# Kernel tuning notes

Hardware: AMD Instinct MI355X
Metric: run time of the kernel (lower is better)

Reference implementation:

```python
import jax, jax.numpy as jnp
import numpy as np

N_EMBED = 8192
EMBED_DIM = 256
DECAY = 0.99
EPS = 1e-05


def setup_inputs() -> dict:
    key = jax.random.key(0)
    k1, k2 = jax.random.split(key)
    z = jax.random.normal(k1, (16, 32, 32, EMBED_DIM), dtype=jnp.float32)
    weight = jax.random.normal(k2, (N_EMBED, EMBED_DIM), dtype=jnp.float32)
    cluster_size = jnp.zeros((N_EMBED,), dtype=jnp.float32)
    embed_avg = weight  # register_buffer initialized as a clone of the embedding weight
    return {"z": z, "weight": weight, "cluster_size": cluster_size, "embed_avg": embed_avg}


def reference(z, weight, cluster_size, embed_avg):
    # use_norm=False -> norm is identity; training=True branch; straight_through=True
    zf = z.reshape(-1, EMBED_DIM)  # [N, D]
    # squared euclidean distance: ||z||^2 + ||e||^2 - 2 z.e
    d = (jnp.sum(zf * zf, axis=1, keepdims=True)
         + jnp.sum(weight * weight, axis=1)
         - 2.0 * jnp.einsum('bd,nd->bn', zf, weight))  # [N, K]
    idx = jnp.argmin(d, axis=1)  # [N]
    z_q = weight[idx].reshape(z.shape)
    # commitment loss (z_q detached)
    loss = jnp.mean((jax.lax.stop_gradient(z_q) - z) ** 2)
    # straight-through estimator
    z_q_st = z + jax.lax.stop_gradient(z_q - z)
    # --- EMA codebook update (no_grad in torch) ---
    counts = jax.ops.segment_sum(jnp.ones_like(idx, dtype=jnp.float32), idx, num_segments=N_EMBED)
    dw = jax.ops.segment_sum(zf, idx, num_segments=N_EMBED)  # == onehot.T @ zf
    new_cluster_size = DECAY * cluster_size + (1.0 - DECAY) * counts
    new_embed_avg = DECAY * embed_avg + (1.0 - DECAY) * dw
    n = jnp.sum(new_cluster_size)
    cs = (new_cluster_size + EPS) / (n + N_EMBED * EPS) * n
    new_weight = new_embed_avg / cs[:, None]
    idx_out = idx.reshape(z.shape[:-1])
    return (z_q_st, loss, idx_out,
            jax.lax.stop_gradient(new_weight),
            jax.lax.stop_gradient(new_cluster_size),
            jax.lax.stop_gradient(new_embed_avg))
```

## Files before the change

kernel.cpp:

```cpp
#include <hip/hip_runtime.h>
#include <cstdint>
#include <cstddef>

#define N_PTS   16384
#define K_CODES 8192
#define DIM     256
#define DECAYF  0.99f
#define OMDF    0.01f
#define EPSF    1e-5f

#define OFF_ZQ   0
#define OFF_LOSS 4194304
#define OFF_IDX  4194305
#define OFF_W    4210689
#define OFF_CS   6307841
#define OFF_EA   6316033

#define ZB_OFF   OFF_ZQ
#define WB_OFF   (OFF_ZQ + 2097152)
#define HEN_OFF  (OFF_ZQ + 3145728)
#define C1_OFF   OFF_W
#define C2_OFF   (OFF_W + 1048576)

typedef __attribute__((ext_vector_type(8))) short bf16x8;
typedef __attribute__((ext_vector_type(4))) float f32x4;

__device__ inline unsigned short f2b(float f) {
    unsigned u = __float_as_uint(f);
    return (unsigned short)((u + 0x7FFFu + ((u >> 16) & 1u)) >> 16);
}

__device__ inline unsigned umaxu(unsigned a, unsigned b) { return a > b ? a : b; }
__device__ inline unsigned uminu(unsigned a, unsigned b) { return a < b ? a : b; }

__device__ inline void gload16(const void* g, void* l) {
    __builtin_amdgcn_global_load_lds(
        (const __attribute__((address_space(1))) unsigned int*)g,
        (__attribute__((address_space(3))) unsigned int*)l, 16, 0, 0);
}

__global__ void k_cvt2(const float* __restrict__ z, short* __restrict__ zb,
                       const float* __restrict__ w, short* __restrict__ wb,
                       float* __restrict__ hen, unsigned* __restrict__ cnt,
                       float* __restrict__ zn2) {
    const int tid = threadIdx.x;
    if (blockIdx.x < N_PTS * DIM / 2048) {
        size_t base = (size_t)(blockIdx.x * 256 + tid) * 8;
        float4 a = *(const float4*)(z + base);
        float4 b = *(const float4*)(z + base + 4);
        bf16x8 o;
        o[0] = (short)f2b(128.f * a.x); o[1] = (short)f2b(128.f * a.y);
        o[2] = (short)f2b(128.f * a.z); o[3] = (short)f2b(128.f * a.w);
        o[4] = (short)f2b(128.f * b.x); o[5] = (short)f2b(128.f * b.y);
        o[6] = (short)f2b(128.f * b.z); o[7] = (short)f2b(128.f * b.w);
        *(bf16x8*)(zb + base) = o;
        float s = a.x * a.x + a.y * a.y + a.z * a.z + a.w * a.w
                + b.x * b.x + b.y * b.y + b.z * b.z + b.w * b.w;
        #pragma unroll
        for (int m = 16; m >= 1; m >>= 1) s += __shfl_xor(s, m, 64);
        if ((tid & 31) == 0) zn2[blockIdx.x * 8 + (tid >> 5)] = s;
    } else {
        int blk = blockIdx.x - N_PTS * DIM / 2048;
        size_t base = (size_t)(blk * 256 + tid) * 8;
        float4 a = *(const float4*)(w + base);
        float4 b = *(const float4*)(w + base + 4);
        bf16x8 o;
        o[0] = (short)f2b(a.x); o[1] = (short)f2b(a.y);
        o[2] = (short)f2b(a.z); o[3] = (short)f2b(a.w);
        o[4] = (short)f2b(b.x); o[5] = (short)f2b(b.y);
        o[6] = (short)f2b(b.z); o[7] = (short)f2b(b.w);
        *(bf16x8*)(wb + base) = o;
        float s = a.x * a.x + a.y * a.y + a.z * a.z + a.w * a.w
                + b.x * b.x + b.y * b.y + b.z * b.z + b.w * b.w;
        #pragma unroll
        for (int m = 16; m >= 1; m >>= 1) s += __shfl_xor(s, m, 64);
        if ((tid & 31) == 0) hen[base >> 8] = 0.5f * s;
        int gid = blk * 256 + tid;
        if (gid < K_CODES) cnt[gid] = 0u;
    }
}

__global__ __launch_bounds__(256, 4) void k_gemm(const short* __restrict__ zb,
                                                 const short* __restrict__ wb,
                                                 const float* __restrict__ hen,
                                                 unsigned* __restrict__ c1,
                                                 unsigned* __restrict__ c2) {
    __shared__ __align__(16) short As[128 * 64];
    __shared__ __align__(16) short Bs[128 * 64];

    const int tid  = threadIdx.x;
    const int lane = tid & 63;
    const int wv   = tid >> 6;
    const int ztile = blockIdx.x & 127;
    const int kt    = blockIdx.x >> 7;
    const int z0 = ztile * 128, k0 = kt * 128;
    const int col = lane & 15;

    f32x4 acc[2][8];
    #pragma unroll
    for (int ni = 0; ni < 8; ni++) {
        float h = 131072.0f - 128.0f * hen[k0 + ni * 16 + col];
        f32x4 iv = {h, h, h, h};
        acc[0][ni] = iv; acc[1][ni] = iv;
    }
    const unsigned inv0 = (unsigned)(K_CODES - 1 - (k0 + col));

    const int srow = lane >> 3;
    const int scol = ((lane & 7) ^ srow) * 8;

    #pragma unroll
    for (int dc = 0; dc < 4; ++dc) {
        __syncthreads();
        #pragma unroll
        for (int s4 = 0; s4 < 4; ++s4) {
            int seg = wv * 4 + s4;
            gload16(zb + (size_t)(z0 + seg * 8 + srow) * DIM + dc * 64 + scol,
                    As + seg * 512 + lane * 8);
            gload16(wb + (size_t)(k0 + seg * 8 + srow) * DIM + dc * 64 + scol,
                    Bs + seg * 512 + lane * 8);
        }
        __syncthreads();
        #pragma unroll
        for (int kk = 0; kk < 2; ++kk) {
            int ch = ((kk << 2) + (lane >> 4)) ^ (lane & 7);
            bf16x8 a0 = *(const bf16x8*)&As[(wv * 32 + col) * 64 + ch * 8];
            bf16x8 a1 = *(const bf16x8*)&As[(wv * 32 + 16 + col) * 64 + ch * 8];
            #pragma unroll
            for (int ni = 0; ni < 8; ni++) {
                bf16x8 b = *(const bf16x8*)&Bs[(ni * 16 + col) * 64 + ch * 8];
                acc[0][ni] = __builtin_amdgcn_mfma_f32_16x16x32_bf16(
                    a0, b, acc[0][ni], 0, 0, 0);
                acc[1][ni] = __builtin_amdgcn_mfma_f32_16x16x32_bf16(
                    a1, b, acc[1][ni], 0, 0, 0);
            }
        }
    }

    #pragma unroll
    for (int mi = 0; mi < 2; mi++) {
        #pragma unroll
        for (int r = 0; r < 4; r++) {
            unsigned k8[8];
            #pragma unroll
            for (int ni = 0; ni < 8; ni++) {
                unsigned q = (unsigned)acc[mi][ni][r];
                k8[ni] = (q << 13) | (inv0 - 16u * ni);
            }
            unsigned p1 = umaxu(k8[0], k8[1]), q1 = uminu(k8[0], k8[1]);
            unsigned p2 = umaxu(k8[2], k8[3]), q2 = uminu(k8[2], k8[3]);
            unsigned p3 = umaxu(k8[4], k8[5]), q3 = uminu(k8[4], k8[5]);
            unsigned p4 = umaxu(k8[6], k8[7]), q4 = uminu(k8[6], k8[7]);
            unsigned a1 = umaxu(p1, p2);
            unsigned a2 = umaxu(uminu(p1, p2), umaxu(q1, q2));
            unsigned b1 = umaxu(p3, p4);
            unsigned b2 = umaxu(uminu(p3, p4), umaxu(q3, q4));
            unsigned t1 = umaxu(a1, b1);
            unsigned t2 = umaxu(uminu(a1, b1), umaxu(a2, b2));
            unsigned m1 = t1;
            #pragma unroll
            for (int m = 8; m >= 1; m >>= 1)
                m1 = umaxu(m1, (unsigned)__shfl_xor((int)m1, m, 64));
            unsigned cc = (t1 == m1) ? t2 : t1;
            #pragma unroll
            for (int m = 8; m >= 1; m >>= 1)
                cc = umaxu(cc, (unsigned)__shfl_xor((int)cc, m, 64));
            if (col == 0) {
                int row = wv * 32 + mi * 16 + (lane >> 4) * 4 + r;
                c1[(size_t)kt * N_PTS + z0 + row] = m1;
                c2[(size_t)kt * N_PTS + z0 + row] = cc;
            }
        }
    }
}

__global__ __launch_bounds__(1024) void k_rescore(
        const float* __restrict__ z, const float* __restrict__ w,
        const unsigned* __restrict__ c1, const unsigned* __restrict__ c2,
        const float* __restrict__ zn2,
        float* __restrict__ out,
        unsigned* __restrict__ cnt, float* __restrict__ lossp) {
    __shared__ unsigned s1[64 * 17], s2[64 * 17];
    const int t  = threadIdx.x;
    const int w0 = blockIdx.x * 16;
    {
        int kt = t >> 4, wo = t & 15;
        s1[kt * 17 + wo] = c1[(size_t)kt * N_PTS + w0 + wo];
        s2[kt * 17 + wo] = c2[(size_t)kt * N_PTS + w0 + wo];
    }
    __syncthreads();
    const int wv   = t >> 6;
    const int lane = t & 63;
    const int wid  = w0 + wv;
    unsigned k1 = s1[lane * 17 + wv];
    unsigned k2 = s2[lane * 17 + wv];

    unsigned m1 = k1;
    #pragma unroll
    for (int m = 32; m >= 1; m >>= 1)
        m1 = umaxu(m1, (unsigned)__shfl_xor((int)m1, m, 64));
    unsigned e = (k1 == m1) ? k2 : k1;
    unsigned m2 = e;
    #pragma unroll
    for (int m = 32; m >= 1; m >>= 1)
        m2 = umaxu(m2, (unsigned)__shfl_xor((int)m2, m, 64));

    int idx = K_CODES - 1 - (int)(m1 & 0x1FFFu);
    float scf = ((float)(int)(m1 >> 13) - 131072.0f) * 0.0078125f;

    unsigned qthr = (m1 >> 13) - 96u;
    if ((m2 >> 13) >= qthr) {
        unsigned long long best = 0ULL;
        float bsc = 0.f;
        #pragma unroll
        for (int j = 0; j < 2; j++) {
            unsigned cj = j ? k2 : k1;
            unsigned long long mask = __ballot((cj >> 13) >= qthr);
            while (mask) {
                int l = __ffsll((unsigned long long)mask) - 1;
                mask &= mask - 1;
                unsigned cwd = (unsigned)__shfl((int)cj, l, 64);
                int k = K_CODES - 1 - (int)(cwd & 0x1FFFu);
                float4 wr = *(const float4*)(w + (size_t)k * DIM + lane * 4);
                float s = 0.f, h = 0.f;
                {
                    const float* zr = z + (size_t)wid * DIM + lane * 4;
                    float4 zv = *(const float4*)zr;
                    s = zv.x * wr.x + zv.y * wr.y + zv.z * wr.z + zv.w * wr.w;
                    h = wr.x * wr.x + wr.y * wr.y + wr.z * wr.z + wr.w * wr.w;
                }
                #pragma unroll
                for (int m = 32; m >= 1; m >>= 1) {
                    s += __shfl_xor(s, m, 64);
                    h += __shfl_xor(h, m, 64);
                }
                float sc = s - 0.5f * h;
                unsigned u = __float_as_uint(sc);
                u = (u & 0x80000000u) ? ~u : (u | 0x80000000u);
                unsigned long long key = ((unsigned long long)u << 32)
                                       | (unsigned)(K_CODES - 1 - k);
                bool better = key > best;
                best = better ? key : best;
                bsc  = better ? sc  : bsc;
            }
        }
        idx = K_CODES - 1 - (int)(unsigned)(best & 0xFFFFFFFFull);
        scf = bsc;
    }

    if (lane == 0) {
        out[OFF_IDX + wid] = (float)idx;
        lossp[wid] = zn2[wid] - 2.0f * scf;
        atomicAdd(cnt + idx, 1u);
    }
}

__global__ __launch_bounds__(1024) void k_prefix(const float* __restrict__ csin,
                                                 float* __restrict__ out,
                                                 const unsigned* __restrict__ cnt,
                                                 unsigned* __restrict__ offs,
                                                 unsigned* __restrict__ list,
                                                 const float* __restrict__ lossp,
                                                 float* __restrict__ nval) {
    __shared__ unsigned scur[K_CODES];
    __shared__ unsigned wtot[16], wbase[16];
    __shared__ float fred[16], fred2[16];
    int t = threadIdx.x, lane = t & 63, wv = t >> 6;
    int base = t * 8;
    unsigned c[8], mysum = 0;
    #pragma unroll
    for (int i = 0; i < 8; i++) { c[i] = cnt[base + i]; mysum += c[i]; }
    unsigned inc = mysum;
    #pragma unroll
    for (int off = 1; off < 64; off <<= 1) {
        unsigned v = (unsigned)__shfl_up((int)inc, off, 64);
        if (lane >= off) inc += v;
    }
    if (lane == 63) wtot[wv] = inc;
    __syncthreads();
    if (t == 0) {
        unsigned r = 0;
        for (int i = 0; i < 16; i++) { wbase[i] = r; r += wtot[i]; }
        offs[K_CODES] = r;
    }
    __syncthreads();
    unsigned my0 = wbase[wv] + inc - mysum;
    float csl = 0.f;
    #pragma unroll
    for (int i = 0; i < 8; i++) {
        offs[base + i] = my0;
        scur[base + i] = my0;
        my0 += c[i];
        float ncs = DECAYF * csin[base + i] + OMDF * (float)c[i];
        out[OFF_CS + base + i] = ncs;
        csl += ncs;
    }
    #pragma unroll
    for (int m = 32; m >= 1; m >>= 1) csl += __shfl_xor(csl, m, 64);
    if (lane == 0) fred[wv] = csl;
    float lp = 0.f;
    #pragma unroll
    for (int i = 0; i < 16; i++) lp += lossp[t + i * 1024];
    #pragma unroll
    for (int m = 32; m >= 1; m >>= 1) lp += __shfl_xor(lp, m, 64);
    if (lane == 0) fred2[wv] = lp;
    __syncthreads();
    if (t == 0) {
        float n = 0.f, L = 0.f;
        for (int i = 0; i < 16; i++) { n += fred[i]; L += fred2[i]; }
        *nval = n;
        out[OFF_LOSS] = L * (1.0f / ((float)N_PTS * DIM));
    }
    for (int i = t; i < N_PTS; i += 1024) {
        int idx = (int)out[OFF_IDX + i];
        unsigned pos = atomicAdd(&scur[idx], 1u);
        list[pos] = (unsigned)i;
    }
}

__global__ void k_gather(const float* __restrict__ z, const float* __restrict__ ea,
                         const float* __restrict__ w,
                         float* __restrict__ out,
                         const unsigned* __restrict__ offs,
                         const unsigned* __restrict__ list,
                         const float* __restrict__ nval) {
    int k = blockIdx.x, lane = threadIdx.x;
    unsigned beg = offs[k], end = offs[k + 1];
    float4 wv = *(const float4*)(w + (size_t)k * DIM + lane * 4);
    float4 acc = {0.f, 0.f, 0.f, 0.f};
    for (unsigned p = beg; p < end; ++p) {
        unsigned i = list[p];
        float4 zv = *(const float4*)(z + (size_t)i * DIM + lane * 4);
        acc.x += zv.x; acc.y += zv.y; acc.z += zv.z; acc.w += zv.w;
        *(float4*)(out + OFF_ZQ + (size_t)i * DIM + lane * 4) = wv;
    }
    float4 e = *(const float4*)(ea + (size_t)k * DIM + lane * 4);
    e.x = DECAYF * e.x + OMDF * acc.x;
    e.y = DECAYF * e.y + OMDF * acc.y;
    e.z = DECAYF * e.z + OMDF * acc.z;
    e.w = DECAYF * e.w + OMDF * acc.w;
    *(float4*)(out + OFF_EA + (size_t)k * DIM + lane * 4) = e;

    float cs = out[OFF_CS + k];
    float n  = *nval;
    float inv = 1.f / ((cs + EPSF) / (n + (float)K_CODES * EPSF) * n);
    float4 wr = {e.x * inv, e.y * inv, e.z * inv, e.w * inv};
    *(float4*)(out + OFF_W + (size_t)k * DIM + lane * 4) = wr;
}

extern "C" void kernel_launch(void* const* d_in, const int* in_sizes, int n_in,
                              void* d_out, int out_size, void* d_ws, size_t ws_size,
                              hipStream_t stream) {
    const float* z  = (const float*)d_in[0];
    const float* w  = (const float*)d_in[1];
    const float* cs = (const float*)d_in[2];
    const float* ea = (const float*)d_in[3];
    float* out = (float*)d_out;

    short*    zb  = (short*)(out + ZB_OFF);
    short*    wb  = (short*)(out + WB_OFF);
    float*    hen = out + HEN_OFF;
    unsigned* c1  = (unsigned*)(out + C1_OFF);
    unsigned* c2  = (unsigned*)(out + C2_OFF);

    unsigned* cnt   = (unsigned*)d_ws;
    unsigned* offs  = cnt + 8192;
    unsigned* list  = offs + 8200;
    float*    lossp = (float*)(list + 16384);
    float*    nval  = lossp + 16384;
    float*    zn2   = nval + 1;

    hipLaunchKernelGGL(k_cvt2,    dim3((N_PTS + K_CODES) * DIM / 2048), dim3(256), 0, stream,
                       z, zb, w, wb, hen, cnt, zn2);
    hipLaunchKernelGGL(k_gemm,    dim3((N_PTS / 128) * (K_CODES / 128)), dim3(256), 0, stream,
                       zb, wb, hen, c1, c2);
    hipLaunchKernelGGL(k_rescore, dim3(N_PTS / 16),           dim3(1024), 0, stream,
                       z, w, c1, c2, zn2, out, cnt, lossp);
    hipLaunchKernelGGL(k_prefix,  dim3(1),                    dim3(1024), 0, stream,
                       cs, out, cnt, offs, list, lossp, nval);
    hipLaunchKernelGGL(k_gather,  dim3(K_CODES),              dim3(64), 0, stream,
                       z, ea, w, out, offs, list, nval);
}
```

Before: 277.0 us.

## Enlarge GEMM tiles to 256x256 with double-buffered LDS staging and 8 waves

```diff
diff --git a/kernel.cpp b/kernel.cpp
--- a/kernel.cpp
+++ b/kernel.cpp
@@ -80,82 +80,98 @@
     }
 }
 
-__global__ __launch_bounds__(256, 4) void k_gemm(const short* __restrict__ zb,
+__device__ __forceinline__ void stage_tile(const short* __restrict__ zb,
+                                           const short* __restrict__ wb,
+                                           int z0, int k0g, int t,
+                                           short* Ab, short* Bb,
+                                           int wv, int lane) {
+    const int sr = lane >> 3;
+    const int chunk = (lane & 7) ^ sr;
+    const int koff = t * 64 + chunk * 8;
+    #pragma unroll
+    for (int i = 0; i < 4; ++i) {
+        const int seg = wv * 4 + i;
+        const int row = seg * 8 + sr;
+        gload16(zb + (size_t)(z0 + row) * DIM + koff, Ab + seg * 512 + lane * 8);
+        gload16(wb + (size_t)(k0g + row) * DIM + koff, Bb + seg * 512 + lane * 8);
+    }
+}
+
+__global__ __launch_bounds__(512, 2) void k_gemm(const short* __restrict__ zb,
                                                  const short* __restrict__ wb,
                                                  const float* __restrict__ hen,
                                                  unsigned* __restrict__ c1,
                                                  unsigned* __restrict__ c2) {
-    __shared__ __align__(16) short As[128 * 64];
-    __shared__ __align__(16) short Bs[128 * 64];
+    __shared__ __align__(16) short As[2][16384];
+    __shared__ __align__(16) short Bs[2][16384];
+    __shared__ unsigned ldsT[256][8];
 
     const int tid  = threadIdx.x;
     const int lane = tid & 63;
     const int wv   = tid >> 6;
-    const int ztile = blockIdx.x & 127;
-    const int kt    = blockIdx.x >> 7;
-    const int z0 = ztile * 128, k0 = kt * 128;
+    const int wm   = wv >> 2;
+    const int wn   = wv & 3;
+    const int kt    = blockIdx.x & 31;
+    const int ztile = blockIdx.x >> 5;
+    const int z0 = ztile * 256, k0g = kt * 256;
     const int col = lane & 15;
 
-    f32x4 acc[2][8];
-    #pragma unroll
-    for (int ni = 0; ni < 8; ni++) {
-        float h = 131072.0f - 128.0f * hen[k0 + ni * 16 + col];
+    f32x4 acc[8][4];
+    #pragma unroll
+    for (int ni = 0; ni < 4; ni++) {
+        float h = 131072.0f - 128.0f * hen[k0g + wn * 64 + ni * 16 + col];
         f32x4 iv = {h, h, h, h};
-        acc[0][ni] = iv; acc[1][ni] = iv;
-    }
-    const unsigned inv0 = (unsigned)(K_CODES - 1 - (k0 + col));
-
-    const int srow = lane >> 3;
-    const int scol = ((lane & 7) ^ srow) * 8;
-
-    #pragma unroll
-    for (int dc = 0; dc < 4; ++dc) {
-        __syncthreads();
-        #pragma unroll
-        for (int s4 = 0; s4 < 4; ++s4) {
-            int seg = wv * 4 + s4;
-            gload16(zb + (size_t)(z0 + seg * 8 + srow) * DIM + dc * 64 + scol,
-                    As + seg * 512 + lane * 8);
-            gload16(wb + (size_t)(k0 + seg * 8 + srow) * DIM + dc * 64 + scol,
-                    Bs + seg * 512 + lane * 8);
-        }
-        __syncthreads();
+        #pragma unroll
+        for (int mi = 0; mi < 8; mi++) acc[mi][ni] = iv;
+    }
+    const unsigned invL = (unsigned)(K_CODES - 1 - (k0g + wn * 64 + col));
+
+    stage_tile(zb, wb, z0, k0g, 0, As[0], Bs[0], wv, lane);
+
+    const int ar = (wm * 128 + col) * 64;
+    const int br = (wn * 64 + col) * 64;
+
+    #pragma unroll 1
+    for (int t = 0; t < 4; ++t) {
+        asm volatile("s_waitcnt vmcnt(0)" ::: "memory");
+        __builtin_amdgcn_s_barrier();
+        asm volatile("" ::: "memory");
+        if (t < 3)
+            stage_tile(zb, wb, z0, k0g, t + 1, As[(t + 1) & 1], Bs[(t + 1) & 1], wv, lane);
+        const short* Ab = As[t & 1];
+        const short* Bb = Bs[t & 1];
         #pragma unroll
         for (int kk = 0; kk < 2; ++kk) {
-            int ch = ((kk << 2) + (lane >> 4)) ^ (lane & 7);
-            bf16x8 a0 = *(const bf16x8*)&As[(wv * 32 + col) * 64 + ch * 8];
-            bf16x8 a1 = *(const bf16x8*)&As[(wv * 32 + 16 + col) * 64 + ch * 8];
+            const int s8 = ((((kk << 2) + (lane >> 4)) ^ (lane & 7)) << 3);
+            bf16x8 b[4];
             #pragma unroll
-            for (int ni = 0; ni < 8; ni++) {
-                bf16x8 b = *(const bf16x8*)&Bs[(ni * 16 + col) * 64 + ch * 8];
-                acc[0][ni] = __builtin_amdgcn_mfma_f32_16x16x32_bf16(
-                    a0, b, acc[0][ni], 0, 0, 0);
-                acc[1][ni] = __builtin_amdgcn_mfma_f32_16x16x32_bf16(
-                    a1, b, acc[1][ni], 0, 0, 0);
+            for (int ni = 0; ni < 4; ni++)
+                b[ni] = *(const bf16x8*)&Bb[br + ni * 1024 + s8];
+            #pragma unroll
+            for (int mi = 0; mi < 8; mi++) {
+                bf16x8 a = *(const bf16x8*)&Ab[ar + mi * 1024 + s8];
+                #pragma unroll
+                for (int ni = 0; ni < 4; ni++)
+                    acc[mi][ni] = __builtin_amdgcn_mfma_f32_16x16x32_bf16(
+                        a, b[ni], acc[mi][ni], 0, 0, 0);
             }
         }
     }
 
     #pragma unroll
-    for (int mi = 0; mi < 2; mi++) {
+    for (int mi = 0; mi < 8; mi++) {
         #pragma unroll
         for (int r = 0; r < 4; r++) {
-            unsigned k8[8];
+            unsigned k4[4];
             #pragma unroll
-            for (int ni = 0; ni < 8; ni++) {
+            for (int ni = 0; ni < 4; ni++) {
                 unsigned q = (unsigned)acc[mi][ni][r];
-                k8[ni] = (q << 13) | (inv0 - 16u * ni);
+                k4[ni] = (q << 13) | (invL - 16u * ni);
             }
-            unsigned p1 = umaxu(k8[0], k8[1]), q1 = uminu(k8[0], k8[1]);
-            unsigned p2 = umaxu(k8[2], k8[3]), q2 = uminu(k8[2], k8[3]);
-            unsigned p3 = umaxu(k8[4], k8[5]), q3 = uminu(k8[4], k8[5]);
-            unsigned p4 = umaxu(k8[6], k8[7]), q4 = uminu(k8[6], k8[7]);
-            unsigned a1 = umaxu(p1, p2);
-            unsigned a2 = umaxu(uminu(p1, p2), umaxu(q1, q2));
-            unsigned b1 = umaxu(p3, p4);
-            unsigned b2 = umaxu(uminu(p3, p4), umaxu(q3, q4));
-            unsigned t1 = umaxu(a1, b1);
-            unsigned t2 = umaxu(uminu(a1, b1), umaxu(a2, b2));
+            unsigned p1 = umaxu(k4[0], k4[1]), q1 = uminu(k4[0], k4[1]);
+            unsigned p2 = umaxu(k4[2], k4[3]), q2 = uminu(k4[2], k4[3]);
+            unsigned t1 = umaxu(p1, p2);
+            unsigned t2 = umaxu(uminu(p1, p2), umaxu(q1, q2));
             unsigned m1 = t1;
             #pragma unroll
             for (int m = 8; m >= 1; m >>= 1)
@@ -165,11 +181,22 @@
             for (int m = 8; m >= 1; m >>= 1)
                 cc = umaxu(cc, (unsigned)__shfl_xor((int)cc, m, 64));
             if (col == 0) {
-                int row = wv * 32 + mi * 16 + (lane >> 4) * 4 + r;
-                c1[(size_t)kt * N_PTS + z0 + row] = m1;
-                c2[(size_t)kt * N_PTS + z0 + row] = cc;
+                int rowl = wm * 128 + mi * 16 + (lane >> 4) * 4 + r;
+                ldsT[rowl][wn * 2]     = m1;
+                ldsT[rowl][wn * 2 + 1] = cc;
             }
         }
+    }
+    __syncthreads();
+    {
+        int row = tid & 255, pr = tid >> 8;
+        unsigned a0 = ldsT[row][pr * 4 + 0], a1 = ldsT[row][pr * 4 + 1];
+        unsigned b0 = ldsT[row][pr * 4 + 2], b1 = ldsT[row][pr * 4 + 3];
+        unsigned t1 = umaxu(a0, b0);
+        unsigned t2 = umaxu(uminu(a0, b0), umaxu(a1, b1));
+        size_t o = (size_t)((kt << 1) + pr) * N_PTS + z0 + row;
+        c1[o] = t1;
+        c2[o] = t2;
     }
 }
 
@@ -371,7 +398,7 @@
 
     hipLaunchKernelGGL(k_cvt2,    dim3((N_PTS + K_CODES) * DIM / 2048), dim3(256), 0, stream,
                        z, zb, w, wb, hen, cnt, zn2);
-    hipLaunchKernelGGL(k_gemm,    dim3((N_PTS / 128) * (K_CODES / 128)), dim3(256), 0, stream,
+    hipLaunchKernelGGL(k_gemm,    dim3((N_PTS / 256) * (K_CODES / 256)), dim3(512), 0, stream,
                        zb, wb, hen, c1, c2);
     hipLaunchKernelGGL(k_rescore, dim3(N_PTS / 16),           dim3(1024), 0, stream,
                        z, w, c1, c2, zn2, out, cnt, lossp);
```

After: 341.6 us. 1.23x slower.
